# Performance work log

Hardware: AMD Instinct MI355X
Metric: run time of the kernel (lower is better)

## Reference

```python
import jax, jax.numpy as jnp
import numpy as np

# Constants from __init__ (domain bounds)
X_MIN, X_MAX = -1.0, 1.0
Y_MIN, Y_MAX = -1.0, 1.0
T_MIN, T_MAX = 0.0, 1.0

N_POINTS = 262144
WIDTH = 128
N_HIDDEN_STACK = 5  # hidden->hidden layers between first and last


def setup_inputs() -> dict:
    key = jax.random.key(0)
    ks = jax.random.split(key, 8)
    X = jax.random.uniform(ks[0], (N_POINTS, 4), dtype=jnp.float32)
    # glorot_normal-ish init
    def glorot(k, fan_in, fan_out, shape):
        std = (2.0 / (fan_in + fan_out)) ** 0.5
        return jax.random.normal(k, shape, dtype=jnp.float32) * std
    W0 = glorot(ks[1], 4, WIDTH, (4, WIDTH))
    b0 = jnp.zeros((WIDTH,), dtype=jnp.float32)
    Wh = glorot(ks[2], WIDTH, WIDTH, (N_HIDDEN_STACK, WIDTH, WIDTH))
    bh = jnp.zeros((N_HIDDEN_STACK, WIDTH), dtype=jnp.float32)
    WL = glorot(ks[3], WIDTH, 2, (WIDTH, 2))
    bL = jnp.zeros((2,), dtype=jnp.float32)
    nu_min = jnp.zeros((), dtype=jnp.float32)
    nu_max = jnp.ones((), dtype=jnp.float32)
    return {"X": X, "nu_min": nu_min, "nu_max": nu_max,
            "W0": W0, "b0": b0, "Wh": Wh, "bh": bh, "WL": WL, "bL": bL}


def _swish(x):
    return x * jax.nn.sigmoid(x)


def reference(X, nu_min, nu_max, W0, b0, Wh, bh, WL, bL):
    # Input rescaling to [-1, 1] per feature, then concat
    x_s = 2.0 * (X[:, 0:1] - X_MIN) / (X_MAX - X_MIN) - 1.0
    y_s = 2.0 * (X[:, 1:2] - Y_MIN) / (Y_MAX - Y_MIN) - 1.0
    t_s = 2.0 * (X[:, 2:3] - T_MIN) / (T_MAX - T_MIN) - 1.0
    nu_s = 2.0 * (X[:, 3:4] - nu_min) / (nu_max - nu_min) - 1.0
    H = jnp.concatenate([x_s, y_s, t_s, nu_s], axis=1)  # [N, 4]
    # Stacked small dense + swish layers (fused-MLP candidate)
    H = _swish(H @ W0 + b0)  # [N, WIDTH]
    for i in range(Wh.shape[0]):
        H = _swish(H @ Wh[i] + bh[i])
    return H @ WL + bL  # [N, 2], no activation on output layer
```

## Files before the change

kernel.cpp:

```cpp
#include <hip/hip_runtime.h>

typedef __bf16 bf16x8 __attribute__((ext_vector_type(8)));
typedef __bf16 bf16x2 __attribute__((ext_vector_type(2)));
typedef float  f32x4  __attribute__((ext_vector_type(4)));

#define WS_WT0_B 0
#define WS_WTH_B 8192
#define WS_WLT_B 172032

__device__ __forceinline__ unsigned short f2b(float f) {
  return __builtin_bit_cast(unsigned short, (__bf16)f);
}

__global__ void prep_kernel(const float* __restrict__ W0,
                            const float* __restrict__ Wh,
                            const float* __restrict__ WL,
                            unsigned short* __restrict__ ws) {
  int i = blockIdx.x * 256 + threadIdx.x;
  int l  = (i >> 3) & 63;
  int j  = i & 7;
  int lm = l & 15, lh = l >> 4;
  if (i < 4096) {
    int nt = i >> 9;
    int n = nt * 16 + lm, k = lh * 8 + j;
    ws[i] = f2b(k < 4 ? W0[k * 128 + n] : 0.f);
  } else if (i < 86016) {
    int t = i - 4096;
    int frag = t >> 9;
    int nt = frag & 7, ks = (frag >> 3) & 3, h = frag >> 5;
    int n = nt * 16 + lm, k = ks * 32 + lh * 8 + j;
    ws[i] = f2b(Wh[(h * 128 + k) * 128 + n]);
  } else if (i < 90112) {
    int t = i - 86016;
    int f = t >> 9;
    int k = (f & 3) * 32 + lh * 8 + j;
    ws[i] = f2b((f < 4 && lm < 2) ? WL[k * 2 + lm] : 0.f);
  }
}

__device__ __forceinline__ f32x4 swish4(f32x4 z) {
  const f32x4 u = z * (-1.44269504088896340736f);
  f32x4 e;
#if __has_builtin(__builtin_amdgcn_exp2f)
  e[0] = __builtin_amdgcn_exp2f(u[0]); e[1] = __builtin_amdgcn_exp2f(u[1]);
  e[2] = __builtin_amdgcn_exp2f(u[2]); e[3] = __builtin_amdgcn_exp2f(u[3]);
#else
  e[0] = __expf(u[0] * 0.6931471805599453f); e[1] = __expf(u[1] * 0.6931471805599453f);
  e[2] = __expf(u[2] * 0.6931471805599453f); e[3] = __expf(u[3] * 0.6931471805599453f);
#endif
  const f32x4 w = e + 1.f;
  f32x4 s;
  s[0] = __builtin_amdgcn_rcpf(w[0]); s[1] = __builtin_amdgcn_rcpf(w[1]);
  s[2] = __builtin_amdgcn_rcpf(w[2]); s[3] = __builtin_amdgcn_rcpf(w[3]);
  return z * s;
}

__device__ __forceinline__ uint2 pack4(f32x4 r) {
  bf16x2 lo = {(__bf16)r[0], (__bf16)r[1]};
  bf16x2 hi = {(__bf16)r[2], (__bf16)r[3]};
  uint2 wv;
  wv.x = __builtin_bit_cast(unsigned int, lo);
  wv.y = __builtin_bit_cast(unsigned int, hi);
  return wv;
}

#define LRD(addr) __builtin_bit_cast(bf16x8, *reinterpret_cast<const uint4*>(addr))
#define MFMA(a, b, c) __builtin_amdgcn_mfma_f32_16x16x32_bf16((a), (b), (c), 0, 0, 0)

__device__ __forceinline__ void stage8k(const char* src, char* dst, int tid) {
  const int woff = (tid >> 6) * 1024;
#if __has_builtin(__builtin_amdgcn_global_load_lds)
  __builtin_amdgcn_global_load_lds(
      (const __attribute__((address_space(1))) unsigned int*)(src + tid * 16),
      (__attribute__((address_space(3))) unsigned int*)(dst + woff), 16, 0, 0);
  __builtin_amdgcn_global_load_lds(
      (const __attribute__((address_space(1))) unsigned int*)(src + 4096 + tid * 16),
      (__attribute__((address_space(3))) unsigned int*)(dst + 4096 + woff), 16, 0, 0);
#else
  const uint4 v0 = *reinterpret_cast<const uint4*>(src + tid * 16);
  const uint4 v1 = *reinterpret_cast<const uint4*>(src + 4096 + tid * 16);
  *reinterpret_cast<uint4*>(dst + tid * 16) = v0;
  *reinterpret_cast<uint4*>(dst + 4096 + tid * 16) = v1;
#endif
}

__launch_bounds__(256, 3)
__global__ void mlp_kernel(const float* __restrict__ X,
                           const float* __restrict__ nu_min_p,
                           const float* __restrict__ nu_max_p,
                           const float* __restrict__ b0,
                           const float* __restrict__ bh,
                           const float* __restrict__ bL,
                           const unsigned short* __restrict__ ws,
                           float* __restrict__ out) {
  __shared__ __align__(16) char smem[32768 + 16384 + 2560];
  const int tid  = threadIdx.x;
  const int lane = tid & 63, wave = tid >> 6;
  char* Hs  = smem + wave * 8192;
  char* wb0 = smem + 32768;
  char* wb1 = smem + 40960;
  float* bias_lds = reinterpret_cast<float*>(smem + 49152);
  const int lm = lane & 15, lh = lane >> 4;
  const int row0 = blockIdx.x * 128 + wave * 32;
  const char* wsb = reinterpret_cast<const char*>(ws);
  const int xorm = (lm & 7) << 4;
  const int va0 = lm * 256 + ((lh * 16) ^ xorm);
  const int va1 = va0 + 4096;
  const int wa0 = lm * 256 + ((lh * 8) ^ xorm);
  const int wa1 = wa0 + 4096;

  stage8k(wsb + WS_WT0_B, wb0, tid);
  f32x4 bv0[8];
#pragma unroll
  for (int nt = 0; nt < 8; ++nt)
    bv0[nt] = *reinterpret_cast<const f32x4*>(b0 + nt * 16 + lh * 4);
#pragma unroll
  for (int i = 0; i < 3; ++i) {
    const int idx = i * 256 + tid;
    if (idx < 640) bias_lds[idx] = bh[idx];
  }
  if (lane < 32) {
    const float4 xv = reinterpret_cast<const float4*>(X)[row0 + lane];
    const float numin = nu_min_p[0], numax = nu_max_p[0];
    const float v0 = xv.x;
    const float v1 = xv.y;
    const float v2 = 2.f * xv.z - 1.f;
    const float v3 = 2.f * (xv.w - numin) / (numax - numin) - 1.f;
    uint4 c0;
    c0.x = (unsigned)f2b(v0) | ((unsigned)f2b(v1) << 16);
    c0.y = (unsigned)f2b(v2) | ((unsigned)f2b(v3) << 16);
    c0.z = 0u; c0.w = 0u;
    const uint4 z4 = make_uint4(0u, 0u, 0u, 0u);
    const int xr = (lane & 7) << 4;
    char* rp = Hs + lane * 256;
    *reinterpret_cast<uint4*>(rp + (0  ^ xr)) = c0;
    *reinterpret_cast<uint4*>(rp + (16 ^ xr)) = z4;
    *reinterpret_cast<uint4*>(rp + (32 ^ xr)) = z4;
    *reinterpret_cast<uint4*>(rp + (48 ^ xr)) = z4;
  }
  __syncthreads();

  f32x4 acc[8][2];
  bf16x8 aa[8];
  const f32x4 zero4 = {0.f, 0.f, 0.f, 0.f};

  stage8k(wsb + WS_WTH_B, wb1, tid);
#pragma unroll
  for (int nt = 0; nt < 8; ++nt) aa[nt] = LRD(wb0 + nt * 1024 + lane * 16);
  {
    const bf16x8 f0 = LRD(Hs + va0);
    const bf16x8 f1 = LRD(Hs + va1);
#pragma unroll
    for (int nt = 0; nt < 8; ++nt) {
      acc[nt][0] = MFMA(aa[nt], f0, bv0[nt]);
      acc[nt][1] = MFMA(aa[nt], f1, bv0[nt]);
    }
  }
#pragma unroll
  for (int nt = 0; nt < 8; ++nt) {
#pragma unroll
    for (int pt = 0; pt < 2; ++pt) {
      const uint2 wv = pack4(swish4(acc[nt][pt]));
      *reinterpret_cast<uint2*>(Hs + ((pt ? wa1 : wa0) ^ (nt << 5))) = wv;
    }
  }
  __syncthreads();

#define HPHASE(RBUF, SBUF, SRC, KSOFF, FIRST)                              \
  do {                                                                     \
    stage8k((SRC), (SBUF), tid);                                           \
    _Pragma("unroll")                                                      \
    for (int nt = 0; nt < 8; ++nt) aa[nt] = LRD((RBUF) + nt * 1024 + lane * 16); \
    const bf16x8 f0 = LRD(Hs + (va0 ^ (KSOFF)));                           \
    const bf16x8 f1 = LRD(Hs + (va1 ^ (KSOFF)));                           \
    _Pragma("unroll")                                                      \
    for (int nt = 0; nt < 8; ++nt) {                                       \
      acc[nt][0] = MFMA(aa[nt], f0, (FIRST) ? zero4 : acc[nt][0]);         \
      acc[nt][1] = MFMA(aa[nt], f1, (FIRST) ? zero4 : acc[nt][1]);         \
    }                                                                      \
  } while (0)

#pragma unroll 1
  for (int h = 0; h < 5; ++h) {
    const char* wsrc = wsb + WS_WTH_B + h * 32768;
    const float* bl = bias_lds + h * 128;
    const char* nsrc = (h < 4) ? (wsrc + 32768) : (wsb + WS_WLT_B);

    HPHASE(wb1, wb0, wsrc + 8192,  0,   true);
    __syncthreads();
    HPHASE(wb0, wb1, wsrc + 16384, 64,  false);
    __syncthreads();
    HPHASE(wb1, wb0, wsrc + 24576, 128, false);
    __syncthreads();
    HPHASE(wb0, wb1, nsrc,         192, false);
#pragma unroll
    for (int nt = 0; nt < 8; ++nt) {
      const f32x4 bv = *reinterpret_cast<const f32x4*>(bl + nt * 16 + lh * 4);
#pragma unroll
      for (int pt = 0; pt < 2; ++pt) {
        const uint2 wv = pack4(swish4(acc[nt][pt] + bv));
        *reinterpret_cast<uint2*>(Hs + ((pt ? wa1 : wa0) ^ (nt << 5))) = wv;
      }
    }
    __syncthreads();
  }

  {
    const float bl0 = bL[0], bl1 = bL[1];
#pragma unroll
    for (int ks = 0; ks < 4; ++ks) aa[ks] = LRD(wb1 + ks * 1024 + lane * 16);
#pragma unroll
    for (int pt = 0; pt < 2; ++pt) {
      f32x4 accL = {0.f, 0.f, 0.f, 0.f};
#pragma unroll
      for (int ks = 0; ks < 4; ++ks) {
        const bf16x8 f = LRD(Hs + ((pt ? va1 : va0) ^ (ks << 6)));
        accL = MFMA(aa[ks], f, accL);
      }
      if (lh == 0) {
        const int p = pt * 16 + lm;
        float2 o;
        o.x = accL[0] + bl0;
        o.y = accL[1] + bl1;
        *reinterpret_cast<float2*>(out + (size_t)(row0 + p) * 2) = o;
      }
    }
  }
#undef HPHASE
}

extern "C" void kernel_launch(void* const* d_in, const int* in_sizes, int n_in,
                              void* d_out, int out_size, void* d_ws, size_t ws_size,
                              hipStream_t stream) {
  const float* X     = (const float*)d_in[0];
  const float* numin = (const float*)d_in[1];
  const float* numax = (const float*)d_in[2];
  const float* W0    = (const float*)d_in[3];
  const float* b0    = (const float*)d_in[4];
  const float* Wh    = (const float*)d_in[5];
  const float* bh    = (const float*)d_in[6];
  const float* WL    = (const float*)d_in[7];
  const float* bL    = (const float*)d_in[8];
  unsigned short* ws = (unsigned short*)d_ws;
  float* out = (float*)d_out;

  hipLaunchKernelGGL(prep_kernel, dim3(352), dim3(256), 0, stream, W0, Wh, WL, ws);
  hipLaunchKernelGGL(mlp_kernel, dim3(2048), dim3(256), 0, stream,
                     X, numin, numax, b0, bh, bL, ws, out);
}
```

Baseline: 76.70 us.

## Split output columns across waves sharing a 64-row activation tile

Restructures the MLP kernel so each block handles 64 rows with a shared activation tile, and each wave computes two 16-column output tiles for all rows instead of all columns for 32 private rows. This cuts LDS and register use to allow four blocks per CU and doubles the grid. In exchange, each row incurs twice the weight staging traffic, and an extra barrier per layer is needed because waves now read and write the shared activation tile.

```diff
diff --git a/kernel.cpp b/kernel.cpp
--- a/kernel.cpp
+++ b/kernel.cpp
@@ -84,7 +84,7 @@
 #endif
 }
 
-__launch_bounds__(256, 3)
+__launch_bounds__(256, 4)
 __global__ void mlp_kernel(const float* __restrict__ X,
                            const float* __restrict__ nu_min_p,
                            const float* __restrict__ nu_max_p,
@@ -93,34 +93,33 @@
                            const float* __restrict__ bL,
                            const unsigned short* __restrict__ ws,
                            float* __restrict__ out) {
-  __shared__ __align__(16) char smem[32768 + 16384 + 2560];
+  __shared__ __align__(16) char smem[16384 + 16384 + 2560];
+  char* Hs  = smem;
+  char* wb0 = smem + 16384;
+  char* wb1 = smem + 24576;
+  float* bias_lds = reinterpret_cast<float*>(smem + 32768);
   const int tid  = threadIdx.x;
   const int lane = tid & 63, wave = tid >> 6;
-  char* Hs  = smem + wave * 8192;
-  char* wb0 = smem + 32768;
-  char* wb1 = smem + 40960;
-  float* bias_lds = reinterpret_cast<float*>(smem + 49152);
   const int lm = lane & 15, lh = lane >> 4;
-  const int row0 = blockIdx.x * 128 + wave * 32;
+  const int row0 = blockIdx.x * 64;
   const char* wsb = reinterpret_cast<const char*>(ws);
   const int xorm = (lm & 7) << 4;
-  const int va0 = lm * 256 + ((lh * 16) ^ xorm);
-  const int va1 = va0 + 4096;
-  const int wa0 = lm * 256 + ((lh * 8) ^ xorm);
-  const int wa1 = wa0 + 4096;
-
-  stage8k(wsb + WS_WT0_B, wb0, tid);
-  f32x4 bv0[8];
-#pragma unroll
-  for (int nt = 0; nt < 8; ++nt)
-    bv0[nt] = *reinterpret_cast<const f32x4*>(b0 + nt * 16 + lh * 4);
+  const int ntb = wave * 2;
+  int vaG[4], waG[4];
+#pragma unroll
+  for (int g = 0; g < 4; ++g) {
+    vaG[g] = (g * 16 + lm) * 256 + ((lh * 16) ^ xorm);
+    waG[g] = (g * 16 + lm) * 256 + (((lh * 8) ^ xorm) ^ (wave << 6));
+  }
+
+  stage8k(wsb + WS_WT0_B, wb1, tid);
 #pragma unroll
   for (int i = 0; i < 3; ++i) {
     const int idx = i * 256 + tid;
     if (idx < 640) bias_lds[idx] = bh[idx];
   }
-  if (lane < 32) {
-    const float4 xv = reinterpret_cast<const float4*>(X)[row0 + lane];
+  if (tid < 64) {
+    const float4 xv = reinterpret_cast<const float4*>(X)[row0 + tid];
     const float numin = nu_min_p[0], numax = nu_max_p[0];
     const float v0 = xv.x;
     const float v1 = xv.y;
@@ -131,8 +130,8 @@
     c0.y = (unsigned)f2b(v2) | ((unsigned)f2b(v3) << 16);
     c0.z = 0u; c0.w = 0u;
     const uint4 z4 = make_uint4(0u, 0u, 0u, 0u);
-    const int xr = (lane & 7) << 4;
-    char* rp = Hs + lane * 256;
+    const int xr = (tid & 7) << 4;
+    char* rp = Hs + tid * 256;
     *reinterpret_cast<uint4*>(rp + (0  ^ xr)) = c0;
     *reinterpret_cast<uint4*>(rp + (16 ^ xr)) = z4;
     *reinterpret_cast<uint4*>(rp + (32 ^ xr)) = z4;
@@ -140,93 +139,89 @@
   }
   __syncthreads();
 
-  f32x4 acc[8][2];
-  bf16x8 aa[8];
-  const f32x4 zero4 = {0.f, 0.f, 0.f, 0.f};
-
-  stage8k(wsb + WS_WTH_B, wb1, tid);
-#pragma unroll
-  for (int nt = 0; nt < 8; ++nt) aa[nt] = LRD(wb0 + nt * 1024 + lane * 16);
+  f32x4 acc[2][4];
+  bf16x8 a0, a1;
+
   {
-    const bf16x8 f0 = LRD(Hs + va0);
-    const bf16x8 f1 = LRD(Hs + va1);
-#pragma unroll
-    for (int nt = 0; nt < 8; ++nt) {
-      acc[nt][0] = MFMA(aa[nt], f0, bv0[nt]);
-      acc[nt][1] = MFMA(aa[nt], f1, bv0[nt]);
+    stage8k(wsb + WS_WTH_B, wb0, tid);
+    a0 = LRD(wb1 + (ntb + 0) * 1024 + lane * 16);
+    a1 = LRD(wb1 + (ntb + 1) * 1024 + lane * 16);
+    const f32x4 bv0 = *reinterpret_cast<const f32x4*>(b0 + (ntb + 0) * 16 + lh * 4);
+    const f32x4 bv1 = *reinterpret_cast<const f32x4*>(b0 + (ntb + 1) * 16 + lh * 4);
+#pragma unroll
+    for (int g = 0; g < 4; ++g) {
+      const bf16x8 f = LRD(Hs + vaG[g]);
+      acc[0][g] = MFMA(a0, f, bv0);
+      acc[1][g] = MFMA(a1, f, bv1);
     }
-  }
-#pragma unroll
-  for (int nt = 0; nt < 8; ++nt) {
-#pragma unroll
-    for (int pt = 0; pt < 2; ++pt) {
-      const uint2 wv = pack4(swish4(acc[nt][pt]));
-      *reinterpret_cast<uint2*>(Hs + ((pt ? wa1 : wa0) ^ (nt << 5))) = wv;
-    }
-  }
-  __syncthreads();
-
-#define HPHASE(RBUF, SBUF, SRC, KSOFF, FIRST)                              \
-  do {                                                                     \
-    stage8k((SRC), (SBUF), tid);                                           \
-    _Pragma("unroll")                                                      \
-    for (int nt = 0; nt < 8; ++nt) aa[nt] = LRD((RBUF) + nt * 1024 + lane * 16); \
-    const bf16x8 f0 = LRD(Hs + (va0 ^ (KSOFF)));                           \
-    const bf16x8 f1 = LRD(Hs + (va1 ^ (KSOFF)));                           \
-    _Pragma("unroll")                                                      \
-    for (int nt = 0; nt < 8; ++nt) {                                       \
-      acc[nt][0] = MFMA(aa[nt], f0, (FIRST) ? zero4 : acc[nt][0]);         \
-      acc[nt][1] = MFMA(aa[nt], f1, (FIRST) ? zero4 : acc[nt][1]);         \
-    }                                                                      \
+    __syncthreads();
+#pragma unroll
+    for (int j = 0; j < 2; ++j)
+#pragma unroll
+      for (int g = 0; g < 4; ++g) {
+        const uint2 wv = pack4(swish4(acc[j][g]));
+        *reinterpret_cast<uint2*>(Hs + (waG[g] ^ (j << 5))) = wv;
+      }
+    __syncthreads();
+  }
+
+#define HPHASE(RBUF, SBUF, SRC, KSOFF, C0, C1)                               \
+  do {                                                                       \
+    stage8k((SRC), (SBUF), tid);                                             \
+    a0 = LRD((RBUF) + (ntb + 0) * 1024 + lane * 16);                         \
+    a1 = LRD((RBUF) + (ntb + 1) * 1024 + lane * 16);                         \
+    _Pragma("unroll")                                                        \
+    for (int g = 0; g < 4; ++g) {                                            \
+      const bf16x8 f = LRD(Hs + (vaG[g] ^ (KSOFF)));                         \
+      acc[0][g] = MFMA(a0, f, (C0));                                         \
+      acc[1][g] = MFMA(a1, f, (C1));                                         \
+    }                                                                        \
   } while (0)
 
 #pragma unroll 1
   for (int h = 0; h < 5; ++h) {
     const char* wsrc = wsb + WS_WTH_B + h * 32768;
-    const float* bl = bias_lds + h * 128;
     const char* nsrc = (h < 4) ? (wsrc + 32768) : (wsb + WS_WLT_B);
-
-    HPHASE(wb1, wb0, wsrc + 8192,  0,   true);
-    __syncthreads();
-    HPHASE(wb0, wb1, wsrc + 16384, 64,  false);
-    __syncthreads();
-    HPHASE(wb1, wb0, wsrc + 24576, 128, false);
-    __syncthreads();
-    HPHASE(wb0, wb1, nsrc,         192, false);
-#pragma unroll
-    for (int nt = 0; nt < 8; ++nt) {
-      const f32x4 bv = *reinterpret_cast<const f32x4*>(bl + nt * 16 + lh * 4);
-#pragma unroll
-      for (int pt = 0; pt < 2; ++pt) {
-        const uint2 wv = pack4(swish4(acc[nt][pt] + bv));
-        *reinterpret_cast<uint2*>(Hs + ((pt ? wa1 : wa0) ^ (nt << 5))) = wv;
+    const f32x4 bv0 = *reinterpret_cast<const f32x4*>(bias_lds + h * 128 + (ntb + 0) * 16 + lh * 4);
+    const f32x4 bv1 = *reinterpret_cast<const f32x4*>(bias_lds + h * 128 + (ntb + 1) * 16 + lh * 4);
+
+    HPHASE(wb0, wb1, wsrc + 8192,  0,   bv0, bv1);
+    __syncthreads();
+    HPHASE(wb1, wb0, wsrc + 16384, 64,  acc[0][g], acc[1][g]);
+    __syncthreads();
+    HPHASE(wb0, wb1, wsrc + 24576, 128, acc[0][g], acc[1][g]);
+    __syncthreads();
+    HPHASE(wb1, wb0, nsrc,         192, acc[0][g], acc[1][g]);
+    __syncthreads();
+#pragma unroll
+    for (int j = 0; j < 2; ++j)
+#pragma unroll
+      for (int g = 0; g < 4; ++g) {
+        const uint2 wv = pack4(swish4(acc[j][g]));
+        *reinterpret_cast<uint2*>(Hs + (waG[g] ^ (j << 5))) = wv;
       }
-    }
-    __syncthreads();
-  }
+    __syncthreads();
+  }
+#undef HPHASE
 
   {
     const float bl0 = bL[0], bl1 = bL[1];
-#pragma unroll
-    for (int ks = 0; ks < 4; ++ks) aa[ks] = LRD(wb1 + ks * 1024 + lane * 16);
-#pragma unroll
-    for (int pt = 0; pt < 2; ++pt) {
-      f32x4 accL = {0.f, 0.f, 0.f, 0.f};
-#pragma unroll
-      for (int ks = 0; ks < 4; ++ks) {
-        const bf16x8 f = LRD(Hs + ((pt ? va1 : va0) ^ (ks << 6)));
-        accL = MFMA(aa[ks], f, accL);
-      }
-      if (lh == 0) {
-        const int p = pt * 16 + lm;
-        float2 o;
-        o.x = accL[0] + bl0;
-        o.y = accL[1] + bl1;
-        *reinterpret_cast<float2*>(out + (size_t)(row0 + p) * 2) = o;
-      }
+    const int vaF = (wave * 16 + lm) * 256 + ((lh * 16) ^ xorm);
+    f32x4 accL = {0.f, 0.f, 0.f, 0.f};
+#pragma unroll
+    for (int ks = 0; ks < 4; ++ks) {
+      const bf16x8 a = LRD(wb0 + ks * 1024 + lane * 16);
+      const bf16x8 f = LRD(Hs + (vaF ^ (ks << 6)));
+      accL = MFMA(a, f, accL);
     }
-  }
-#undef HPHASE
+    if (lh == 0) {
+      const int p = wave * 16 + lm;
+      float2 o;
+      o.x = accL[0] + bl0;
+      o.y = accL[1] + bl1;
+      *reinterpret_cast<float2*>(out + (size_t)(row0 + p) * 2) = o;
+    }
+  }
 }
 
 extern "C" void kernel_launch(void* const* d_in, const int* in_sizes, int n_in,
@@ -245,6 +240,6 @@
   float* out = (float*)d_out;
 
   hipLaunchKernelGGL(prep_kernel, dim3(352), dim3(256), 0, stream, W0, Wh, WL, ws);
-  hipLaunchKernelGGL(mlp_kernel, dim3(2048), dim3(256), 0, stream,
+  hipLaunchKernelGGL(mlp_kernel, dim3(4096), dim3(256), 0, stream,
                      X, numin, numax, b0, bh, bL, ws, out);
 }
```

Result: slower. 78.77 us (+2.7%).
